# Optimization experiments

Hardware: AMD Instinct MI355X
Metric: run time of the kernel (lower is better)

The kernel has to match this reference:

```python
import jax, jax.numpy as jnp
import numpy as np

EPS = 1e-6

def rmsnorm(x, w):
    # x * rsqrt(mean(x^2, -1) + eps) * w
    ms = jnp.mean(jnp.square(x), axis=-1, keepdims=True)
    return w * (x * jax.lax.rsqrt(ms + EPS))

def setup_inputs() -> dict:
    key = jax.random.key(0)
    ks = jax.random.split(key, 10)
    B, L, T, D, R = 4, 8, 2048, 1024, 64
    h_base = jax.random.normal(ks[0], (B, T, D), dtype=jnp.float32)
    prev_states = jax.random.normal(ks[1], (B, L, T, D), dtype=jnp.float32)
    query = jax.random.normal(ks[2], (D,), dtype=jnp.float32) * 0.02
    gate = jnp.float32(0.5)
    score_w = jnp.ones((D,), dtype=jnp.float32)
    out_w = jnp.ones((D,), dtype=jnp.float32)
    qnorm_w = jnp.ones((D,), dtype=jnp.float32)
    # low-rank query projections (nn.Linear weight layout: [out, in])
    Wd = jax.random.normal(ks[3], (R, D), dtype=jnp.float32) * 0.02
    Wu = jax.random.normal(ks[4], (D, R), dtype=jnp.float32) * 0.02
    # token gate projection
    tg_w = jax.random.normal(ks[5], (1, D), dtype=jnp.float32) * 0.02
    tg_b = jnp.zeros((1,), dtype=jnp.float32)
    return {"h_base": h_base, "prev_states": prev_states, "query": query,
            "gate": gate, "score_w": score_w, "out_w": out_w,
            "qnorm_w": qnorm_w, "Wd": Wd, "Wu": Wu, "tg_w": tg_w, "tg_b": tg_b}

def reference(h_base, prev_states, query, gate, score_w, out_w, qnorm_w, Wd, Wu, tg_w, tg_b):
    sources = prev_states                              # [B,L,T,D]
    normed = rmsnorm(sources, score_w)                 # [B,L,T,D]
    # low-rank input-dependent query: q = query + up(down(qnorm(h)))
    qh = rmsnorm(h_base, qnorm_w)                      # [B,T,D]
    q = query + jnp.einsum('btr,dr->btd', jnp.einsum('btd,rd->btr', qh, Wd), Wu)
    scores = jnp.einsum('btd,bltd->blt', q, normed)    # [B,L,T]
    alpha = jax.nn.softmax(scores, axis=1)             # softmax over depth L
    delta = jnp.einsum('blt,bltd->btd', alpha, sources)
    delta = rmsnorm(delta, out_w)                      # [B,T,D]
    g = gate * jax.nn.sigmoid(h_base @ tg_w.T + tg_b)  # [B,T,1]
    out = h_base + g * delta
    return out, alpha
```

## Files before the change

### kernel.cpp

```cpp
#include <hip/hip_runtime.h>
#include <hip/hip_bf16.h>

#define D_DIM 1024
#define L_DIM 8
#define T_DIM 2048
#define B_DIM 4
#define TOKS  (B_DIM * T_DIM)
#define OUT_ELEMS ((size_t)TOKS * D_DIM)
#define EPSF 1e-6f

typedef __attribute__((ext_vector_type(8)))  short short8_t;
typedef __attribute__((ext_vector_type(16))) float f32x16_t;
typedef __attribute__((ext_vector_type(4)))  float f32x4_t;

__device__ __forceinline__ float dot4v(const f32x4_t& a, const f32x4_t& b) {
    return a.x * b.x + a.y * b.y + a.z * b.z + a.w * b.w;
}

__device__ __forceinline__ unsigned short f2bf(float f) {
    union { __hip_bfloat16 h; unsigned short u; } x;
    x.h = __float2bfloat16(f);
    return x.u;
}

__device__ __forceinline__ float bf2f(unsigned short u) {
    union { unsigned int i; float f; } x;
    x.i = ((unsigned int)u) << 16;
    return x.f;
}

__global__ __launch_bounds__(512) void k_all(const float* __restrict__ h,
                                             const float* __restrict__ prev,
                                             const float* __restrict__ query,
                                             const float* __restrict__ score_w,
                                             const float* __restrict__ out_w,
                                             const float* __restrict__ tg_w,
                                             const float* __restrict__ gate,
                                             const float* __restrict__ tg_b,
                                             const float* __restrict__ qnw,
                                             const float* __restrict__ Wd,
                                             const float* __restrict__ Wu,
                                             float* __restrict__ out,
                                             float* __restrict__ alpha_out) {
    __shared__ __align__(16) char smem[65536];
    float (*c_red)[2][16][64] = (float (*)[2][16][64])smem;
    unsigned short* qt = (unsigned short*)smem;

    __shared__ float ssq_red[8][32];
    __shared__ float scale_sh[32];
    __shared__ unsigned short r_sw[2048];

    int tid  = threadIdx.x;
    int w    = tid >> 6;
    int lane = tid & 63;
    int t0   = blockIdx.x * 32;

    f32x16_t acc0, acc1;
#pragma unroll
    for (int r = 0; r < 16; ++r) { acc0[r] = 0.f; acc1[r] = 0.f; }

    int arow = lane & 31;
    int koff = w * 128 + (lane >> 5) * 8;
    const float* hrow = h + (size_t)(t0 + arow) * D_DIM + koff;
    const float* w0r  = Wd + (size_t)arow * D_DIM + koff;
    const float* w1r  = Wd + (size_t)(32 + arow) * D_DIM + koff;
    const float* nr   = qnw + koff;

    float ssq = 0.f;
#pragma unroll
    for (int s = 0; s < 8; ++s) {
        f32x4_t ha = *(const f32x4_t*)(hrow + s * 16);
        f32x4_t hb = *(const f32x4_t*)(hrow + s * 16 + 4);
        ssq += dot4v(ha, ha) + dot4v(hb, hb);
        short8_t af;
        af[0] = (short)f2bf(ha.x); af[1] = (short)f2bf(ha.y);
        af[2] = (short)f2bf(ha.z); af[3] = (short)f2bf(ha.w);
        af[4] = (short)f2bf(hb.x); af[5] = (short)f2bf(hb.y);
        af[6] = (short)f2bf(hb.z); af[7] = (short)f2bf(hb.w);
        f32x4_t na = *(const f32x4_t*)(nr + s * 16);
        f32x4_t nb = *(const f32x4_t*)(nr + s * 16 + 4);
        f32x4_t wa = *(const f32x4_t*)(w0r + s * 16);
        f32x4_t wb = *(const f32x4_t*)(w0r + s * 16 + 4);
        short8_t bf0;
        bf0[0] = (short)f2bf(wa.x * na.x); bf0[1] = (short)f2bf(wa.y * na.y);
        bf0[2] = (short)f2bf(wa.z * na.z); bf0[3] = (short)f2bf(wa.w * na.w);
        bf0[4] = (short)f2bf(wb.x * nb.x); bf0[5] = (short)f2bf(wb.y * nb.y);
        bf0[6] = (short)f2bf(wb.z * nb.z); bf0[7] = (short)f2bf(wb.w * nb.w);
        f32x4_t va = *(const f32x4_t*)(w1r + s * 16);
        f32x4_t vb = *(const f32x4_t*)(w1r + s * 16 + 4);
        short8_t bf1;
        bf1[0] = (short)f2bf(va.x * na.x); bf1[1] = (short)f2bf(va.y * na.y);
        bf1[2] = (short)f2bf(va.z * na.z); bf1[3] = (short)f2bf(va.w * na.w);
        bf1[4] = (short)f2bf(vb.x * nb.x); bf1[5] = (short)f2bf(vb.y * nb.y);
        bf1[6] = (short)f2bf(vb.z * nb.z); bf1[7] = (short)f2bf(vb.w * nb.w);
        acc0 = __builtin_amdgcn_mfma_f32_32x32x16_bf16(af, bf0, acc0, 0, 0, 0);
        acc1 = __builtin_amdgcn_mfma_f32_32x32x16_bf16(af, bf1, acc1, 0, 0, 0);
    }

    ssq += __shfl_xor(ssq, 32, 64);
    if (lane < 32) ssq_red[w][lane] = ssq;
#pragma unroll
    for (int r = 0; r < 16; ++r) {
        c_red[w][0][r][lane] = acc0[r];
        c_red[w][1][r][lane] = acc1[r];
    }
    __syncthreads();

    if (tid < 32) {
        float s8 = 0.f;
#pragma unroll
        for (int u = 0; u < 8; ++u) s8 += ssq_red[u][tid];
        scale_sh[tid] = rsqrtf(s8 * (1.f / D_DIM) + EPSF);
    }
    __syncthreads();

    for (int idx = tid; idx < 2048; idx += 512) {
        int nj = idx >> 10, rem = idx & 1023, reg = rem >> 6, ln = rem & 63;
        float v = 0.f;
#pragma unroll
        for (int u = 0; u < 8; ++u) v += c_red[u][nj][reg][ln];
        int tk = (reg & 3) + 8 * (reg >> 2) + 4 * (ln >> 5);
        int j  = nj * 32 + (ln & 31);
        v *= scale_sh[tk];
        int byte = (tk * 128 + j * 2) ^ ((tk & 7) << 4);
        r_sw[byte >> 1] = f2bf(v);
    }
    __syncthreads();

    short8_t afr[4];
#pragma unroll
    for (int s = 0; s < 4; ++s) {
        int tk = lane & 31;
        int k  = s * 16 + (lane >> 5) * 8;
        int byte = (tk * 128 + k * 2) ^ ((tk & 7) << 4);
        afr[s] = *(const short8_t*)(&r_sw[byte >> 1]);
    }
    __syncthreads();

#pragma unroll
    for (int i = 0; i < 4; ++i) {
        int n0 = (w * 4 + i) * 32;
        int d  = n0 + (lane & 31);
        f32x16_t c;
#pragma unroll
        for (int r = 0; r < 16; ++r) c[r] = 0.f;
        const float* wup = Wu + (size_t)d * 64 + (lane >> 5) * 8;
#pragma unroll
        for (int s = 0; s < 4; ++s) {
            f32x4_t ua = *(const f32x4_t*)(wup + s * 16);
            f32x4_t ub = *(const f32x4_t*)(wup + s * 16 + 4);
            short8_t bf;
            bf[0] = (short)f2bf(ua.x); bf[1] = (short)f2bf(ua.y);
            bf[2] = (short)f2bf(ua.z); bf[3] = (short)f2bf(ua.w);
            bf[4] = (short)f2bf(ub.x); bf[5] = (short)f2bf(ub.y);
            bf[6] = (short)f2bf(ub.z); bf[7] = (short)f2bf(ub.w);
            c = __builtin_amdgcn_mfma_f32_32x32x16_bf16(afr[s], bf, c, 0, 0, 0);
        }
        float qd  = query[d];
        float swd = score_w[d];
#pragma unroll
        for (int r = 0; r < 16; ++r) {
            int tk = (r & 3) + 8 * (r >> 2) + 4 * (lane >> 5);
            unsigned int v = f2bf((qd + c[r]) * swd);
            unsigned int pv = (unsigned int)__shfl_xor((int)v, 1, 64);
            if ((lane & 1) == 0) {
                unsigned int word = (v & 0xffffu) | (pv << 16);
                *(unsigned int*)&qt[tk * 1024 + d] = word;
            }
        }
    }
    __syncthreads();

    int bb    = t0 >> 11;
    int tloc0 = t0 & (T_DIM - 1);

#pragma unroll 1
    for (int i = 0; i < 4; ++i) {
        int tt  = w * 4 + i;
        int tok = t0 + tt;
        int t   = tloc0 + tt;

        const float* pb = prev + ((size_t)(bb * L_DIM) * T_DIM + t) * D_DIM + lane * 4;
        f32x4_t p[L_DIM][4];
#pragma unroll
        for (int l = 0; l < L_DIM; ++l)
#pragma unroll
            for (int c = 0; c < 4; ++c)
                p[l][c] = *(const f32x4_t*)(pb + (size_t)l * T_DIM * D_DIM + c * 256);

        const float* hb = h + (size_t)tok * D_DIM + lane * 4;
        f32x4_t h4[4], qv[4];
#pragma unroll
        for (int c = 0; c < 4; ++c) h4[c] = *(const f32x4_t*)(hb + c * 256);
#pragma unroll
        for (int c = 0; c < 4; ++c) {
            short4 qr = *(const short4*)&qt[tt * 1024 + c * 256 + lane * 4];
            qv[c].x = bf2f((unsigned short)qr.x);
            qv[c].y = bf2f((unsigned short)qr.y);
            qv[c].z = bf2f((unsigned short)qr.z);
            qv[c].w = bf2f((unsigned short)qr.w);
        }

        float tgp = 0.f;
#pragma unroll
        for (int c = 0; c < 4; ++c) {
            f32x4_t tw = *(const f32x4_t*)(tg_w + c * 256 + lane * 4);
            tgp += dot4v(h4[c], tw);
        }

        float ss[L_DIM], dt[L_DIM];
#pragma unroll
        for (int l = 0; l < L_DIM; ++l) {
            float s = 0.f, d = 0.f;
#pragma unroll
            for (int c = 0; c < 4; ++c) {
                s += dot4v(p[l][c], p[l][c]);
                d += dot4v(p[l][c], qv[c]);
            }
            ss[l] = s; dt[l] = d;
        }

#pragma unroll
        for (int off = 32; off; off >>= 1) {
#pragma unroll
            for (int l = 0; l < L_DIM; ++l) {
                ss[l] += __shfl_xor(ss[l], off, 64);
                dt[l] += __shfl_xor(dt[l], off, 64);
            }
            tgp += __shfl_xor(tgp, off, 64);
        }

        float al[L_DIM], mx = -1e30f;
#pragma unroll
        for (int l = 0; l < L_DIM; ++l) {
            al[l] = dt[l] * rsqrtf(ss[l] * (1.f / D_DIM) + EPSF);
            mx = fmaxf(mx, al[l]);
        }
        float asum = 0.f;
#pragma unroll
        for (int l = 0; l < L_DIM; ++l) { al[l] = __expf(al[l] - mx); asum += al[l]; }
        float inv = 1.f / asum;
#pragma unroll
        for (int l = 0; l < L_DIM; ++l) al[l] *= inv;

        float g = gate[0] / (1.f + __expf(-(tgp + tg_b[0])));

        f32x4_t dl[4];
#pragma unroll
        for (int c = 0; c < 4; ++c) { dl[c].x = 0.f; dl[c].y = 0.f; dl[c].z = 0.f; dl[c].w = 0.f; }
#pragma unroll
        for (int l = 0; l < L_DIM; ++l)
#pragma unroll
            for (int c = 0; c < 4; ++c) {
                dl[c].x += al[l] * p[l][c].x;
                dl[c].y += al[l] * p[l][c].y;
                dl[c].z += al[l] * p[l][c].z;
                dl[c].w += al[l] * p[l][c].w;
            }

        float dss = 0.f;
#pragma unroll
        for (int c = 0; c < 4; ++c) dss += dot4v(dl[c], dl[c]);
#pragma unroll
        for (int off = 32; off; off >>= 1) dss += __shfl_xor(dss, off, 64);
        float dscale = rsqrtf(dss * (1.f / D_DIM) + EPSF);

        float* ob = out + (size_t)tok * D_DIM + lane * 4;
#pragma unroll
        for (int c = 0; c < 4; ++c) {
            f32x4_t ow = *(const f32x4_t*)(out_w + c * 256 + lane * 4);
            f32x4_t o;
            o.x = h4[c].x + g * dl[c].x * dscale * ow.x;
            o.y = h4[c].y + g * dl[c].y * dscale * ow.y;
            o.z = h4[c].z + g * dl[c].z * dscale * ow.z;
            o.w = h4[c].w + g * dl[c].w * dscale * ow.w;
            __builtin_nontemporal_store(o, (f32x4_t*)(ob + c * 256));
        }

        if (lane < L_DIM)
            alpha_out[(size_t)bb * (L_DIM * T_DIM) + (size_t)lane * T_DIM + t] = al[lane];
    }
}

extern "C" void kernel_launch(void* const* d_in, const int* in_sizes, int n_in,
                              void* d_out, int out_size, void* d_ws, size_t ws_size,
                              hipStream_t stream) {
    (void)in_sizes; (void)n_in; (void)out_size; (void)d_ws; (void)ws_size;
    const float* h       = (const float*)d_in[0];
    const float* prev    = (const float*)d_in[1];
    const float* query   = (const float*)d_in[2];
    const float* gate    = (const float*)d_in[3];
    const float* score_w = (const float*)d_in[4];
    const float* out_w   = (const float*)d_in[5];
    const float* qnw     = (const float*)d_in[6];
    const float* Wd      = (const float*)d_in[7];
    const float* Wu      = (const float*)d_in[8];
    const float* tg_w    = (const float*)d_in[9];
    const float* tg_b    = (const float*)d_in[10];

    float* out   = (float*)d_out;
    float* alpha = out + OUT_ELEMS;

    k_all<<<TOKS / 32, 512, 0, stream>>>(h, prev, query, score_w, out_w, tg_w,
                                         gate, tg_b, qnw, Wd, Wu, out, alpha);
}
```

Measured before the change: 79.46 us.

## Double-buffer prev loads per layer and keep layers packed as bf16 in registers

Replaces the up-front load of all eight prev layers with a two-buffer software pipeline: one layer's loads are issued while the previous layer's norm and dot are computed, and the next token's first layer is prefetched. Each wave visits layers in a rotated order to spread memory traffic, and the alpha write index is remapped to match. Loaded layers are kept as packed bf16 for the weighted sum, which cuts register pressure but adds rounding error to delta. The pipeline also lowers the number of loads in flight per wave, which may reduce memory-level parallelism.

```diff
diff --git a/kernel.cpp b/kernel.cpp
--- a/kernel.cpp
+++ b/kernel.cpp
@@ -8,6 +8,7 @@
 #define TOKS  (B_DIM * T_DIM)
 #define OUT_ELEMS ((size_t)TOKS * D_DIM)
 #define EPSF 1e-6f
+#define PSTRIDE ((size_t)T_DIM * D_DIM)
 
 typedef __attribute__((ext_vector_type(8)))  short short8_t;
 typedef __attribute__((ext_vector_type(16))) float f32x16_t;
@@ -28,6 +29,37 @@
     x.i = ((unsigned int)u) << 16;
     return x.f;
 }
+
+__device__ __forceinline__ float lo2f(unsigned int u) {
+    union { unsigned int i; float f; } x;
+    x.i = u << 16;
+    return x.f;
+}
+
+__device__ __forceinline__ float hi2f(unsigned int u) {
+    union { unsigned int i; float f; } x;
+    x.i = u & 0xffff0000u;
+    return x.f;
+}
+
+#define ISSUE(BUF, PTR) { const float* _p = (PTR);        \
+    BUF[0] = *(const f32x4_t*)(_p);                       \
+    BUF[1] = *(const f32x4_t*)(_p + 256);                 \
+    BUF[2] = *(const f32x4_t*)(_p + 512);                 \
+    BUF[3] = *(const f32x4_t*)(_p + 768); }
+
+#define PACK2(x, y) ((unsigned int)f2bf(x) | ((unsigned int)f2bf(y) << 16))
+
+#define PROC(S, BUF) {                                                        \
+    float _s = dot4v(BUF[0],BUF[0]) + dot4v(BUF[1],BUF[1])                    \
+             + dot4v(BUF[2],BUF[2]) + dot4v(BUF[3],BUF[3]);                   \
+    float _d = dot4v(BUF[0],qv[0]) + dot4v(BUF[1],qv[1])                      \
+             + dot4v(BUF[2],qv[2]) + dot4v(BUF[3],qv[3]);                     \
+    ss[S] = _s; dt[S] = _d;                                                   \
+    pw[S][0]=PACK2(BUF[0].x,BUF[0].y); pw[S][1]=PACK2(BUF[0].z,BUF[0].w);     \
+    pw[S][2]=PACK2(BUF[1].x,BUF[1].y); pw[S][3]=PACK2(BUF[1].z,BUF[1].w);     \
+    pw[S][4]=PACK2(BUF[2].x,BUF[2].y); pw[S][5]=PACK2(BUF[2].z,BUF[2].w);     \
+    pw[S][6]=PACK2(BUF[3].x,BUF[3].y); pw[S][7]=PACK2(BUF[3].z,BUF[3].w); }
 
 __global__ __launch_bounds__(512) void k_all(const float* __restrict__ h,
                                              const float* __restrict__ prev,
@@ -66,12 +98,12 @@
     const float* w1r  = Wd + (size_t)(32 + arow) * D_DIM + koff;
     const float* nr   = qnw + koff;
 
-    float ssq = 0.f;
+    float ssqa = 0.f;
 #pragma unroll
     for (int s = 0; s < 8; ++s) {
         f32x4_t ha = *(const f32x4_t*)(hrow + s * 16);
         f32x4_t hb = *(const f32x4_t*)(hrow + s * 16 + 4);
-        ssq += dot4v(ha, ha) + dot4v(hb, hb);
+        ssqa += dot4v(ha, ha) + dot4v(hb, hb);
         short8_t af;
         af[0] = (short)f2bf(ha.x); af[1] = (short)f2bf(ha.y);
         af[2] = (short)f2bf(ha.z); af[3] = (short)f2bf(ha.w);
@@ -97,8 +129,8 @@
         acc1 = __builtin_amdgcn_mfma_f32_32x32x16_bf16(af, bf1, acc1, 0, 0, 0);
     }
 
-    ssq += __shfl_xor(ssq, 32, 64);
-    if (lane < 32) ssq_red[w][lane] = ssq;
+    ssqa += __shfl_xor(ssqa, 32, 64);
+    if (lane < 32) ssq_red[w][lane] = ssqa;
 #pragma unroll
     for (int r = 0; r < 16; ++r) {
         c_red[w][0][r][lane] = acc0[r];
@@ -173,23 +205,32 @@
 
     int bb    = t0 >> 11;
     int tloc0 = t0 & (T_DIM - 1);
+    int tt0   = w * 4;
+
+    size_t ro0 = (size_t)((0 + w) & 7) * PSTRIDE;
+    size_t ro1 = (size_t)((1 + w) & 7) * PSTRIDE;
+    size_t ro2 = (size_t)((2 + w) & 7) * PSTRIDE;
+    size_t ro3 = (size_t)((3 + w) & 7) * PSTRIDE;
+    size_t ro4 = (size_t)((4 + w) & 7) * PSTRIDE;
+    size_t ro5 = (size_t)((5 + w) & 7) * PSTRIDE;
+    size_t ro6 = (size_t)((6 + w) & 7) * PSTRIDE;
+    size_t ro7 = (size_t)((7 + w) & 7) * PSTRIDE;
+
+    const float* pb0 = prev + ((size_t)(bb * L_DIM) * T_DIM + (tloc0 + tt0)) * D_DIM + lane * 4;
+
+    f32x4_t bufA[4], bufB[4];
+    ISSUE(bufA, pb0 + ro0);
 
 #pragma unroll 1
     for (int i = 0; i < 4; ++i) {
-        int tt  = w * 4 + i;
+        int tt  = tt0 + i;
         int tok = t0 + tt;
         int t   = tloc0 + tt;
-
-        const float* pb = prev + ((size_t)(bb * L_DIM) * T_DIM + t) * D_DIM + lane * 4;
-        f32x4_t p[L_DIM][4];
-#pragma unroll
-        for (int l = 0; l < L_DIM; ++l)
-#pragma unroll
-            for (int c = 0; c < 4; ++c)
-                p[l][c] = *(const f32x4_t*)(pb + (size_t)l * T_DIM * D_DIM + c * 256);
-
+        const float* pbi = pb0 + (size_t)i * D_DIM;
+        const float* pbn = pb0 + (size_t)(i < 3 ? i + 1 : i) * D_DIM;
+
+        f32x4_t h4[4], qv[4];
         const float* hb = h + (size_t)tok * D_DIM + lane * 4;
-        f32x4_t h4[4], qv[4];
 #pragma unroll
         for (int c = 0; c < 4; ++c) h4[c] = *(const f32x4_t*)(hb + c * 256);
 #pragma unroll
@@ -201,6 +242,18 @@
             qv[c].w = bf2f((unsigned short)qr.w);
         }
 
+        float ss[8], dt[8];
+        unsigned int pw[8][8];
+
+        ISSUE(bufB, pbi + ro1); PROC(0, bufA);
+        ISSUE(bufA, pbi + ro2); PROC(1, bufB);
+        ISSUE(bufB, pbi + ro3); PROC(2, bufA);
+        ISSUE(bufA, pbi + ro4); PROC(3, bufB);
+        ISSUE(bufB, pbi + ro5); PROC(4, bufA);
+        ISSUE(bufA, pbi + ro6); PROC(5, bufB);
+        ISSUE(bufB, pbi + ro7); PROC(6, bufA);
+        ISSUE(bufA, pbn + ro0); PROC(7, bufB);
+
         float tgp = 0.f;
 #pragma unroll
         for (int c = 0; c < 4; ++c) {
@@ -208,40 +261,28 @@
             tgp += dot4v(h4[c], tw);
         }
 
-        float ss[L_DIM], dt[L_DIM];
-#pragma unroll
-        for (int l = 0; l < L_DIM; ++l) {
-            float s = 0.f, d = 0.f;
-#pragma unroll
-            for (int c = 0; c < 4; ++c) {
-                s += dot4v(p[l][c], p[l][c]);
-                d += dot4v(p[l][c], qv[c]);
-            }
-            ss[l] = s; dt[l] = d;
-        }
-
 #pragma unroll
         for (int off = 32; off; off >>= 1) {
 #pragma unroll
-            for (int l = 0; l < L_DIM; ++l) {
+            for (int l = 0; l < 8; ++l) {
                 ss[l] += __shfl_xor(ss[l], off, 64);
                 dt[l] += __shfl_xor(dt[l], off, 64);
             }
             tgp += __shfl_xor(tgp, off, 64);
         }
 
-        float al[L_DIM], mx = -1e30f;
-#pragma unroll
-        for (int l = 0; l < L_DIM; ++l) {
+        float al[8], mx = -1e30f;
+#pragma unroll
+        for (int l = 0; l < 8; ++l) {
             al[l] = dt[l] * rsqrtf(ss[l] * (1.f / D_DIM) + EPSF);
             mx = fmaxf(mx, al[l]);
         }
         float asum = 0.f;
 #pragma unroll
-        for (int l = 0; l < L_DIM; ++l) { al[l] = __expf(al[l] - mx); asum += al[l]; }
+        for (int l = 0; l < 8; ++l) { al[l] = __expf(al[l] - mx); asum += al[l]; }
         float inv = 1.f / asum;
 #pragma unroll
-        for (int l = 0; l < L_DIM; ++l) al[l] *= inv;
+        for (int l = 0; l < 8; ++l) al[l] *= inv;
 
         float g = gate[0] / (1.f + __expf(-(tgp + tg_b[0])));
 
@@ -249,14 +290,17 @@
 #pragma unroll
         for (int c = 0; c < 4; ++c) { dl[c].x = 0.f; dl[c].y = 0.f; dl[c].z = 0.f; dl[c].w = 0.f; }
 #pragma unroll
-        for (int l = 0; l < L_DIM; ++l)
+        for (int l = 0; l < 8; ++l) {
+            float a = al[l];
 #pragma unroll
             for (int c = 0; c < 4; ++c) {
-                dl[c].x += al[l] * p[l][c].x;
-                dl[c].y += al[l] * p[l][c].y;
-                dl[c].z += al[l] * p[l][c].z;
-                dl[c].w += al[l] * p[l][c].w;
+                unsigned int w0 = pw[l][2 * c], w1 = pw[l][2 * c + 1];
+                dl[c].x += a * lo2f(w0);
+                dl[c].y += a * hi2f(w0);
+                dl[c].z += a * lo2f(w1);
+                dl[c].w += a * hi2f(w1);
             }
+        }
 
         float dss = 0.f;
 #pragma unroll
@@ -278,7 +322,8 @@
         }
 
         if (lane < L_DIM)
-            alpha_out[(size_t)bb * (L_DIM * T_DIM) + (size_t)lane * T_DIM + t] = al[lane];
+            alpha_out[(size_t)bb * (L_DIM * T_DIM) +
+                      (size_t)((lane + w) & 7) * T_DIM + t] = al[lane];
     }
 }
 
```

After: 93.10 us. 1.17x slower.
